# Kernel optimization log

Hardware: AMD Instinct MI355X
Metric: run time of the kernel (lower is better)

## Reference

```python
import jax, jax.numpy as jnp
import numpy as np

D_MODEL = 1024
NUM_HEADS = 16
HEAD_DIM = D_MODEL // NUM_HEADS


def setup_inputs() -> dict:
    key = jax.random.key(0)
    ks = jax.random.split(key, 12)
    B, S, D = 4, 2048, D_MODEL
    s = 1.0 / np.sqrt(D)
    return {
        "query": jax.random.normal(ks[0], (B, S, D), jnp.float32),
        "key": jax.random.normal(ks[1], (B, S, D), jnp.float32),
        "value": jax.random.normal(ks[2], (B, S, D), jnp.float32),
        "Wq": jax.random.normal(ks[3], (D, D), jnp.float32) * s,
        "bq": jax.random.normal(ks[4], (D,), jnp.float32) * 0.02,
        "Wk": jax.random.normal(ks[5], (D, D), jnp.float32) * s,
        "bk": jax.random.normal(ks[6], (D,), jnp.float32) * 0.02,
        "Wv": jax.random.normal(ks[7], (D, D), jnp.float32) * s,
        "bv": jax.random.normal(ks[8], (D,), jnp.float32) * 0.02,
        "Wo": jax.random.normal(ks[9], (D, D), jnp.float32) * s,
        "bo": jax.random.normal(ks[10], (D,), jnp.float32) * 0.02,
    }


def _split_heads(x):
    B, S, D = x.shape
    return x.reshape(B, S, NUM_HEADS, HEAD_DIM).transpose(0, 2, 1, 3)  # [B,H,S,hd]


def reference(query, key, value, Wq, bq, Wk, bk, Wv, bv, Wo, bo):
    q = _split_heads(query @ Wq + bq)
    k = _split_heads(key @ Wk + bk)
    v = _split_heads(value @ Wv + bv)
    # NOTE: original scales by 1/sqrt(d_model), not 1/sqrt(head_dim)
    scale = 1.0 / np.sqrt(D_MODEL).astype(np.float32)
    scores = jnp.einsum('bhqd,bhkd->bhqk', q, k) * scale  # [B,H,S,S]
    attn = jax.nn.softmax(scores, axis=-1)
    out = jnp.einsum('bhqk,bhkd->bhqd', attn, v)  # [B,H,S,hd]
    B, H, S, hd = out.shape
    out = out.transpose(0, 2, 1, 3).reshape(B, S, D_MODEL)
    out = out @ Wo + bo
    return out, attn
```

## Files before the change

### kernel.cpp

```cpp
#include <hip/hip_runtime.h>
#include <hip/hip_bf16.h>

typedef __bf16 bf16;
typedef __bf16 bf16x8 __attribute__((ext_vector_type(8)));
typedef __bf16 bf16x4 __attribute__((ext_vector_type(4)));
typedef __bf16 bf16x2 __attribute__((ext_vector_type(2)));
typedef float  f32x4  __attribute__((ext_vector_type(4)));
typedef float  f32x16 __attribute__((ext_vector_type(16)));
typedef unsigned int u32;

#define MFMA(A, B, C)   __builtin_amdgcn_mfma_f32_16x16x32_bf16((A), (B), (C), 0, 0, 0)
#define MFMA32(A, B, C) __builtin_amdgcn_mfma_f32_32x32x16_bf16((A), (B), (C), 0, 0, 0)

static constexpr int BATCH = 4, S = 2048, D = 1024, NH = 16, HD = 64;
static constexpr int M = BATCH * S;
static constexpr float KL = 0.045084220027780106f;

__device__ __forceinline__ void gload16(const void* g, void* l) {
  __builtin_amdgcn_global_load_lds(
      (const __attribute__((address_space(1))) void*)g,
      (__attribute__((address_space(3))) void*)l, 16, 0, 0);
}

__device__ __forceinline__ float fexp2(float x) {
#if __has_builtin(__builtin_amdgcn_exp2f)
  return __builtin_amdgcn_exp2f(x);
#else
  return exp2f(x);
#endif
}

__device__ __forceinline__ u32 pack2(float a, float b) {
  union { bf16x2 h; u32 u; } c;
  c.h = (bf16x2){(bf16)a, (bf16)b};
  return c.u;
}

union U4 { u32 w[4]; bf16x8 v; };

#define WAITV_BAR(n)                                        \
  asm volatile("s_waitcnt vmcnt(" #n ")" ::: "memory");     \
  __builtin_amdgcn_s_barrier();                             \
  __builtin_amdgcn_sched_barrier(0);

__global__ __launch_bounds__(256) void wt_convert(
    const float* __restrict__ W0, const float* __restrict__ W1,
    const float* __restrict__ W2, const float* __restrict__ W3,
    bf16* __restrict__ WtAll)
{
  const float* W = blockIdx.y == 0 ? W0 : blockIdx.y == 1 ? W1
                 : blockIdx.y == 2 ? W2 : W3;
  bf16* dst = WtAll + (size_t)blockIdx.y * (D * D);
  int k0 = (blockIdx.x >> 4) * 64, n0 = (blockIdx.x & 15) * 64;
  __shared__ __align__(16) bf16 T[64][72];
  int tid = threadIdx.x;
#pragma unroll
  for (int i = 0; i < 4; ++i) {
    int c = tid + i * 256, r = c >> 4, seg = c & 15;
    float4 v = *reinterpret_cast<const float4*>(W + (size_t)(k0 + r) * D + n0 + seg * 4);
    T[seg * 4 + 0][r] = (bf16)v.x; T[seg * 4 + 1][r] = (bf16)v.y;
    T[seg * 4 + 2][r] = (bf16)v.z; T[seg * 4 + 3][r] = (bf16)v.w;
  }
  __syncthreads();
#pragma unroll
  for (int i = 0; i < 2; ++i) {
    int c = tid + i * 256, r = c >> 3, seg = c & 7;
    *reinterpret_cast<bf16x8*>(dst + (size_t)(n0 + r) * D + k0 + seg * 8) =
        *reinterpret_cast<const bf16x8*>(&T[r][seg * 8]);
  }
}

__global__ __launch_bounds__(256) void x_convert(
    const float* __restrict__ X0, const float* __restrict__ X1,
    const float* __restrict__ X2, bf16* __restrict__ Y)
{
  int t = blockIdx.y;
  const float* X = t == 0 ? X0 : t == 1 ? X1 : X2;
  bf16* Yp = Y + (size_t)t * M * D;
  int idx = blockIdx.x * 256 + threadIdx.x;
#pragma unroll
  for (int i = 0; i < 4; ++i) {
    size_t j = (size_t)idx + (size_t)i * 524288;
    float4 v = reinterpret_cast<const float4*>(X)[j];
    bf16x4 o; o[0] = (bf16)v.x; o[1] = (bf16)v.y; o[2] = (bf16)v.z; o[3] = (bf16)v.w;
    reinterpret_cast<bf16x4*>(Yp)[j] = o;
  }
}

__global__ __launch_bounds__(256) void qkv_gemm(
    const bf16* __restrict__ Xb, const bf16* __restrict__ WtAll,
    const float* __restrict__ bq, const float* __restrict__ bk, const float* __restrict__ bv,
    bf16* __restrict__ Qb, bf16* __restrict__ Kb, bf16* __restrict__ Vtb)
{
  int v = blockIdx.y;
  const bf16*  X    = Xb + (size_t)v * M * D;
  const bf16*  Wt   = WtAll + (size_t)v * (D * D);
  const float* bias = v == 0 ? bq : v == 1 ? bk : bv;

  int x = blockIdx.x;
  int swz = (x & 7) * 64 + (x >> 3);
  int mt = swz >> 3, nt = swz & 7;
  int m0 = mt * 128, n0 = nt * 128;
  int tid = threadIdx.x, lane = tid & 63, w = tid >> 6;
  int wm = (w >> 1) * 64, wn = (w & 1) * 64;
  int lr = lane & 15, lg = lane >> 4;

  __shared__ __align__(16) unsigned char smem[34816];
  auto As = reinterpret_cast<bf16(*)[128][32]>(smem);
  auto Bs = reinterpret_cast<bf16(*)[128][32]>(smem + 16384);

  f32x4 acc[4][4] = {};

  int srow = w * 32 + (lane >> 2);
  int scol = (lane & 3) * 8;

  auto stage = [&](int buf, int ks) {
    const bf16* ga = X + (size_t)(m0 + srow) * D + ks * 32 + scol;
    bf16* la = &As[buf][w * 32][0];
    gload16(ga, la);
    gload16(ga + 16 * D, la + 16 * 32);
    const bf16* gb = Wt + (size_t)(n0 + srow) * D + ks * 32 + scol;
    bf16* lb = &Bs[buf][w * 32][0];
    gload16(gb, lb);
    gload16(gb + 16 * D, lb + 16 * 32);
  };

  stage(0, 0);
  for (int ks = 0; ks < 32; ++ks) {
    __syncthreads();
    if (ks < 31) stage((ks + 1) & 1, ks + 1);
    int buf = ks & 1;
    bf16x8 af[4], bfr[4];
#pragma unroll
    for (int i = 0; i < 4; ++i)
      af[i] = *reinterpret_cast<const bf16x8*>(&As[buf][wm + i * 16 + lr][8 * lg]);
#pragma unroll
    for (int j = 0; j < 4; ++j)
      bfr[j] = *reinterpret_cast<const bf16x8*>(&Bs[buf][wn + j * 16 + lr][8 * lg]);
#pragma unroll
    for (int i = 0; i < 4; ++i)
#pragma unroll
      for (int j = 0; j < 4; ++j)
        acc[i][j] = MFMA(af[i], bfr[j], acc[i][j]);
  }
  __syncthreads();

  if (v < 2) {
    bf16* Out = v == 0 ? Qb : Kb;
    float qs = v == 0 ? KL : 1.0f;
    auto Es = reinterpret_cast<bf16(*)[128]>(smem);
#pragma unroll
    for (int i = 0; i < 4; ++i)
#pragma unroll
      for (int j = 0; j < 4; ++j) {
        int n = wn + j * 16 + lr;
        float bias_n = bias[n0 + n];
#pragma unroll
        for (int r = 0; r < 4; ++r)
          Es[wm + i * 16 + 4 * lg + r][n] = (bf16)((acc[i][j][r] + bias_n) * qs);
      }
    __syncthreads();
#pragma unroll
    for (int i = 0; i < 8; ++i) {
      int c = tid + i * 256, r = c >> 4, seg = c & 15;
      int mg = m0 + r, b = mg >> 11, s = mg & 2047;
      int ng = n0 + seg * 8, h = ng >> 6, d = ng & 63;
      *reinterpret_cast<bf16x8*>(Out + (((size_t)(b * NH + h)) * S + s) * HD + d) =
          *reinterpret_cast<const bf16x8*>(&Es[r][seg * 8]);
    }
  } else {
    auto Es = reinterpret_cast<bf16(*)[136]>(smem);
#pragma unroll
    for (int i = 0; i < 4; ++i)
#pragma unroll
      for (int j = 0; j < 4; ++j) {
        int n = wn + j * 16 + lr;
        float bias_n = bias[n0 + n];
        bf16x4 t;
#pragma unroll
        for (int r = 0; r < 4; ++r) t[r] = (bf16)(acc[i][j][r] + bias_n);
        *reinterpret_cast<bf16x4*>(&Es[n][wm + i * 16 + 4 * lg]) = t;
      }
    __syncthreads();
#pragma unroll
    for (int i = 0; i < 8; ++i) {
      int c = tid + i * 256, r = c >> 4, seg = c & 15;
      int ng = n0 + r, h = ng >> 6, d = ng & 63;
      int mg = m0 + seg * 8, b = mg >> 11, s = mg & 2047;
      *reinterpret_cast<bf16x8*>(Vtb + (((size_t)(b * NH + h)) * HD + d) * S + s) =
          *reinterpret_cast<const bf16x8*>(&Es[r][seg * 8]);
    }
  }
}

__global__ __launch_bounds__(256) void attn_kernel(
    const bf16* __restrict__ Qb, const bf16* __restrict__ Kb, const bf16* __restrict__ Vtb,
    float* __restrict__ attn_out, bf16* __restrict__ ctx)
{
  int xx = blockIdx.x;
  int xcd = xx & 7, r8 = xx >> 3;
  int bh = xcd + 8 * (r8 >> 5);
  int qb = r8 & 31;
  int tid = threadIdx.x, lane = tid & 63, w = tid >> 6;
  int q32 = lane & 31, hi = lane >> 5;
  int qh = w & 1, kh = w >> 1;

  __shared__ __align__(16) bf16 Ks[2][64][64];
  __shared__ __align__(16) bf16 Vs[2][64][64];
  __shared__ __align__(16) float Ps[64][68];
  __shared__ float sums[2][64];

  int q_row = qb * 64 + qh * 32 + q32;
  const bf16* Qrow = Qb + ((size_t)bh * S + q_row) * HD;
  bf16x8 qreg[4];
#pragma unroll
  for (int c = 0; c < 4; ++c)
    qreg[c] = *reinterpret_cast<const bf16x8*>(Qrow + c * 16 + 8 * hi);

  auto stageK = [&](int buf, int kc) {
    const bf16* base = Kb + ((size_t)bh * S + kc * 64) * HD;
#pragma unroll
    for (int i = 0; i < 2; ++i) {
      int c = i * 256 + tid, row = c >> 3, j = c & 7;
      gload16(base + row * HD + 8 * (j ^ (row & 7)),
              reinterpret_cast<bf16*>(&Ks[buf][0][0]) + c * 8);
    }
  };
  auto stageV = [&](int buf, int kc) {
    const bf16* base = Vtb + (size_t)bh * HD * S + kc * 64;
#pragma unroll
    for (int i = 0; i < 2; ++i) {
      int c = i * 256 + tid, row = c >> 3, j = c & 7;
      gload16(base + (size_t)row * S + 8 * (j ^ (row & 7)),
              reinterpret_cast<bf16*>(&Vs[buf][0][0]) + c * 8);
    }
  };

  int krow = kh * 32 + q32, ks7 = krow & 7;

  float lrun = 0.f;
  stageK(0, 0);
  for (int kc = 0; kc < 32; ++kc) {
    if (kc < 31) {
      stageK((kc + 1) & 1, kc + 1);
      WAITV_BAR(2)
    } else {
      WAITV_BAR(0)
    }
    int buf = kc & 1;
    f32x16 sa = {};
#pragma unroll
    for (int c = 0; c < 4; ++c) {
      bf16x8 kf = *reinterpret_cast<const bf16x8*>(&Ks[buf][krow][8 * ((2 * c + hi) ^ ks7)]);
      sa = MFMA32(kf, qreg[c], sa);
    }
#pragma unroll
    for (int r = 0; r < 16; ++r) lrun += fexp2(sa[r]);
    __builtin_amdgcn_s_barrier();
  }
  lrun += __shfl_xor(lrun, 32);
  if (hi == 0) sums[kh][qh * 32 + q32] = lrun;
  __syncthreads();
  float lg2l = __log2f(sums[0][qh * 32 + q32] + sums[1][qh * 32 + q32]);

  f32x16 oaccA = {}, oaccB = {};
  float* ablk = attn_out + ((size_t)bh * S + qb * 64) * S;

  auto computeB = [&](int buf) {
    f32x16 sa = {};
#pragma unroll
    for (int c = 0; c < 4; ++c) {
      bf16x8 kf = *reinterpret_cast<const bf16x8*>(&Ks[buf][krow][8 * ((2 * c + hi) ^ ks7)]);
      sa = MFMA32(kf, qreg[c], sa);
    }
    u32 pku[8];
#pragma unroll
    for (int rq = 0; rq < 4; ++rq) {
      f32x4 pv;
#pragma unroll
      for (int j = 0; j < 4; ++j) pv[j] = fexp2(sa[rq * 4 + j] - lg2l);
      *reinterpret_cast<f32x4*>(&Ps[qh * 32 + q32][kh * 32 + 8 * rq + 4 * hi]) = pv;
      pku[rq * 2 + 0] = pack2(pv[0], pv[1]);
      pku[rq * 2 + 1] = pack2(pv[2], pv[3]);
    }
#pragma unroll
    for (int c2 = 0; c2 < 2; ++c2) {
      u32 myw0 = hi ? pku[4 * c2 + 2] : pku[4 * c2 + 0];
      u32 myw1 = hi ? pku[4 * c2 + 3] : pku[4 * c2 + 1];
      u32 sdw0 = hi ? pku[4 * c2 + 0] : pku[4 * c2 + 2];
      u32 sdw1 = hi ? pku[4 * c2 + 1] : pku[4 * c2 + 3];
      u32 r0 = __shfl_xor(sdw0, 32);
      u32 r1 = __shfl_xor(sdw1, 32);
      U4 f;
      f.w[0] = hi ? r0 : myw0;
      f.w[1] = hi ? r1 : myw1;
      f.w[2] = hi ? myw0 : r0;
      f.w[3] = hi ? myw1 : r1;
      {
        int vrow = q32, vs7 = vrow & 7;
        bf16x8 vf = *reinterpret_cast<const bf16x8*>(
            &Vs[buf][vrow][8 * ((4 * kh + 2 * c2 + hi) ^ vs7)]);
        oaccA = MFMA32(f.v, vf, oaccA);
      }
      {
        int vrow = 32 + q32, vs7 = vrow & 7;
        bf16x8 vf = *reinterpret_cast<const bf16x8*>(
            &Vs[buf][vrow][8 * ((4 * kh + 2 * c2 + hi) ^ vs7)]);
        oaccB = MFMA32(f.v, vf, oaccB);
      }
    }
  };

  int prow = tid >> 2, pc0 = (tid & 3) * 4;
  auto storeP = [&](int kc) {
    float* dst = ablk + (size_t)prow * S + kc * 64 + pc0;
#pragma unroll
    for (int i = 0; i < 4; ++i)
      __builtin_nontemporal_store(
          *reinterpret_cast<const f32x4*>(&Ps[prow][pc0 + 16 * i]),
          reinterpret_cast<f32x4*>(dst + 16 * i));
  };

  stageK(0, 0); stageV(0, 0);
  stageK(1, 1); stageV(1, 1);
  WAITV_BAR(4)
  computeB(0);
  __builtin_amdgcn_s_barrier();
  storeP(0);

  for (int kc = 1; kc < 32; ++kc) {
    if (kc < 31) {
      stageK((kc + 1) & 1, kc + 1);
      stageV((kc + 1) & 1, kc + 1);
      WAITV_BAR(8)
    } else {
      WAITV_BAR(4)
    }
    computeB(kc & 1);
    __builtin_amdgcn_s_barrier();
    storeP(kc);
  }

  float* fbuf = reinterpret_cast<float*>(&Ks[0][0][0]);
  if (kh == 1) {
#pragma unroll
    for (int reg = 0; reg < 16; ++reg) {
      int qloc = (reg & 3) + 8 * (reg >> 2) + 4 * hi;
      fbuf[(qh * 32 + qloc) * 64 + q32]      = oaccA[reg];
      fbuf[(qh * 32 + qloc) * 64 + 32 + q32] = oaccB[reg];
    }
  }
  __syncthreads();
  bf16* cs = reinterpret_cast<bf16*>(&Vs[0][0][0]);
  if (kh == 0) {
#pragma unroll
    for (int reg = 0; reg < 16; ++reg) {
      int qloc = (reg & 3) + 8 * (reg >> 2) + 4 * hi;
      cs[(qh * 32 + qloc) * 72 + q32] =
          (bf16)(oaccA[reg] + fbuf[(qh * 32 + qloc) * 64 + q32]);
      cs[(qh * 32 + qloc) * 72 + 32 + q32] =
          (bf16)(oaccB[reg] + fbuf[(qh * 32 + qloc) * 64 + 32 + q32]);
    }
  }
  __syncthreads();
  {
    int b = bh >> 4, h = bh & 15;
    int row = tid >> 2, cseg = (tid & 3) * 16;
    bf16* cp = ctx + ((size_t)b * S + qb * 64 + row) * D + h * HD + cseg;
    *reinterpret_cast<bf16x8*>(cp) =
        *reinterpret_cast<const bf16x8*>(&cs[row * 72 + cseg]);
    *reinterpret_cast<bf16x8*>(cp + 8) =
        *reinterpret_cast<const bf16x8*>(&cs[row * 72 + cseg + 8]);
  }
}

__global__ __launch_bounds__(256) void out_gemm(
    const bf16* __restrict__ ctx, const bf16* __restrict__ Wto,
    const float* __restrict__ bo, float* __restrict__ Out)
{
  int x = blockIdx.x;
  int swz = (x & 7) * 64 + (x >> 3);
  int mt = swz >> 3, nt = swz & 7;
  int m0 = mt * 128, n0 = nt * 128;
  int tid = threadIdx.x, lane = tid & 63, w = tid >> 6;
  int wm = (w >> 1) * 64, wn = (w & 1) * 64;
  int lr = lane & 15, lg = lane >> 4;

  __shared__ __align__(16) bf16 As[2][128][32];
  __shared__ __align__(16) bf16 Bs[2][128][32];

  f32x4 acc[4][4] = {};

  int srow = w * 32 + (lane >> 2);
  int scol = (lane & 3) * 8;

  auto stage = [&](int buf, int ks) {
    const bf16* ga = ctx + (size_t)(m0 + srow) * D + ks * 32 + scol;
    bf16* la = &As[buf][w * 32][0];
    gload16(ga, la);
    gload16(ga + 16 * D, la + 16 * 32);
    const bf16* gb = Wto + (size_t)(n0 + srow) * D + ks * 32 + scol;
    bf16* lb = &Bs[buf][w * 32][0];
    gload16(gb, lb);
    gload16(gb + 16 * D, lb + 16 * 32);
  };

  stage(0, 0);
  for (int ks = 0; ks < 32; ++ks) {
    __syncthreads();
    if (ks < 31) stage((ks + 1) & 1, ks + 1);
    int buf = ks & 1;
    bf16x8 af[4], bfr[4];
#pragma unroll
    for (int i = 0; i < 4; ++i)
      af[i] = *reinterpret_cast<const bf16x8*>(&As[buf][wm + i * 16 + lr][8 * lg]);
#pragma unroll
    for (int j = 0; j < 4; ++j)
      bfr[j] = *reinterpret_cast<const bf16x8*>(&Bs[buf][wn + j * 16 + lr][8 * lg]);
#pragma unroll
    for (int i = 0; i < 4; ++i)
#pragma unroll
      for (int j = 0; j < 4; ++j)
        acc[i][j] = MFMA(af[i], bfr[j], acc[i][j]);
  }

#pragma unroll
  for (int i = 0; i < 4; ++i)
#pragma unroll
    for (int j = 0; j < 4; ++j) {
      int n = n0 + wn + j * 16 + lr;
      float bias_n = bo[n];
#pragma unroll
      for (int r = 0; r < 4; ++r)
        Out[(size_t)(m0 + wm + i * 16 + 4 * lg + r) * D + n] = acc[i][j][r] + bias_n;
    }
}

extern "C" void kernel_launch(void* const* d_in, const int* in_sizes, int n_in,
                              void* d_out, int out_size, void* d_ws, size_t ws_size,
                              hipStream_t stream)
{
  const float* query = (const float*)d_in[0];
  const float* key   = (const float*)d_in[1];
  const float* value = (const float*)d_in[2];
  const float* Wq = (const float*)d_in[3]; const float* bq = (const float*)d_in[4];
  const float* Wk = (const float*)d_in[5]; const float* bk = (const float*)d_in[6];
  const float* Wv = (const float*)d_in[7]; const float* bv = (const float*)d_in[8];
  const float* Wo = (const float*)d_in[9]; const float* bo = (const float*)d_in[10];

  float* out  = (float*)d_out;
  float* attn = out + (size_t)M * D;

  char* ws = (char*)d_ws;
  const size_t MiB = 1048576;
  bf16* WtAll = (bf16*)ws;
  bf16* Xb    = (bf16*)(ws + 8 * MiB);
  bf16* Qb    = (bf16*)(ws + 56 * MiB);
  bf16* Kb    = (bf16*)(ws + 72 * MiB);
  bf16* Vtb   = (bf16*)(ws + 88 * MiB);
  bf16* ctx   = Xb;

  wt_convert<<<dim3(256, 4), 256, 0, stream>>>(Wq, Wk, Wv, Wo, WtAll);
  x_convert<<<dim3(2048, 3), 256, 0, stream>>>(query, key, value, Xb);
  qkv_gemm<<<dim3(512, 3), 256, 0, stream>>>(Xb, WtAll, bq, bk, bv, Qb, Kb, Vtb);
  attn_kernel<<<dim3(2048), 256, 0, stream>>>(Qb, Kb, Vtb, attn, ctx);
  out_gemm<<<dim3(512), 256, 0, stream>>>(ctx, WtAll + (size_t)3 * D * D, bo, out);
}
```

Before: 442.4 us.

## Process two query tiles per attention block, fusing second tile's sum pass

Each attention block now handles 128 query rows as two 64-row tiles. The softmax-denominator pass for the second tile is folded into the first tile's output pass, so the K tiles loaded there serve both tiles. This removes one of the four separate K sweeps per pair of tiles and halves the grid to 1024 blocks. The cost is more registers (two Q register sets, more accumulators), less parallelism across blocks, and extra barriers and lgkmcnt waits from the new fence macro.

```diff
diff --git a/kernel.cpp b/kernel.cpp
--- a/kernel.cpp
+++ b/kernel.cpp
@@ -38,9 +38,14 @@
 
 union U4 { u32 w[4]; bf16x8 v; };
 
-#define WAITV_BAR(n)                                        \
-  asm volatile("s_waitcnt vmcnt(" #n ")" ::: "memory");     \
-  __builtin_amdgcn_s_barrier();                             \
+#define WAITV_BAR(n)                                                     \
+  asm volatile("s_waitcnt vmcnt(" #n ") lgkmcnt(0)" ::: "memory");       \
+  __builtin_amdgcn_s_barrier();                                          \
+  __builtin_amdgcn_sched_barrier(0);
+
+#define FENCE_BAR                                                        \
+  asm volatile("s_waitcnt lgkmcnt(0)" ::: "memory");                     \
+  __builtin_amdgcn_s_barrier();                                          \
   __builtin_amdgcn_sched_barrier(0);
 
 __global__ __launch_bounds__(256) void wt_convert(
@@ -199,8 +204,8 @@
 {
   int xx = blockIdx.x;
   int xcd = xx & 7, r8 = xx >> 3;
-  int bh = xcd + 8 * (r8 >> 5);
-  int qb = r8 & 31;
+  int bh = xcd + 8 * (r8 >> 4);
+  int qp = r8 & 15;
   int tid = threadIdx.x, lane = tid & 63, w = tid >> 6;
   int q32 = lane & 31, hi = lane >> 5;
   int qh = w & 1, kh = w >> 1;
@@ -210,12 +215,15 @@
   __shared__ __align__(16) float Ps[64][68];
   __shared__ float sums[2][64];
 
-  int q_row = qb * 64 + qh * 32 + q32;
-  const bf16* Qrow = Qb + ((size_t)bh * S + q_row) * HD;
-  bf16x8 qreg[4];
-#pragma unroll
-  for (int c = 0; c < 4; ++c)
-    qreg[c] = *reinterpret_cast<const bf16x8*>(Qrow + c * 16 + 8 * hi);
+  int qrowX = qp * 128 + qh * 32 + q32;
+  const bf16* QrowX = Qb + ((size_t)bh * S + qrowX) * HD;
+  const bf16* QrowY = QrowX + (size_t)64 * HD;
+  bf16x8 qregX[4], qregY[4];
+#pragma unroll
+  for (int c = 0; c < 4; ++c) {
+    qregX[c] = *reinterpret_cast<const bf16x8*>(QrowX + c * 16 + 8 * hi);
+    qregY[c] = *reinterpret_cast<const bf16x8*>(QrowY + c * 16 + 8 * hi);
+  }
 
   auto stageK = [&](int buf, int kc) {
     const bf16* base = Kb + ((size_t)bh * S + kc * 64) * HD;
@@ -238,7 +246,7 @@
 
   int krow = kh * 32 + q32, ks7 = krow & 7;
 
-  float lrun = 0.f;
+  float xs[4] = {0.f, 0.f, 0.f, 0.f};
   stageK(0, 0);
   for (int kc = 0; kc < 32; ++kc) {
     if (kc < 31) {
@@ -252,37 +260,36 @@
 #pragma unroll
     for (int c = 0; c < 4; ++c) {
       bf16x8 kf = *reinterpret_cast<const bf16x8*>(&Ks[buf][krow][8 * ((2 * c + hi) ^ ks7)]);
-      sa = MFMA32(kf, qreg[c], sa);
-    }
-#pragma unroll
-    for (int r = 0; r < 16; ++r) lrun += fexp2(sa[r]);
-    __builtin_amdgcn_s_barrier();
-  }
-  lrun += __shfl_xor(lrun, 32);
-  if (hi == 0) sums[kh][qh * 32 + q32] = lrun;
+      sa = MFMA32(kf, qregX[c], sa);
+    }
+#pragma unroll
+    for (int r = 0; r < 16; ++r) xs[r & 3] += fexp2(sa[r]);
+    FENCE_BAR
+  }
+  {
+    float lrun = (xs[0] + xs[1]) + (xs[2] + xs[3]);
+    lrun += __shfl_xor(lrun, 32);
+    if (hi == 0) sums[kh][qh * 32 + q32] = lrun;
+  }
   __syncthreads();
-  float lg2l = __log2f(sums[0][qh * 32 + q32] + sums[1][qh * 32 + q32]);
+  float lg2lX = __log2f(sums[0][qh * 32 + q32] + sums[1][qh * 32 + q32]);
 
   f32x16 oaccA = {}, oaccB = {};
-  float* ablk = attn_out + ((size_t)bh * S + qb * 64) * S;
-
-  auto computeB = [&](int buf) {
-    f32x16 sa = {};
-#pragma unroll
-    for (int c = 0; c < 4; ++c) {
-      bf16x8 kf = *reinterpret_cast<const bf16x8*>(&Ks[buf][krow][8 * ((2 * c + hi) ^ ks7)]);
-      sa = MFMA32(kf, qreg[c], sa);
-    }
-    u32 pku[8];
-#pragma unroll
-    for (int rq = 0; rq < 4; ++rq) {
-      f32x4 pv;
-#pragma unroll
-      for (int j = 0; j < 4; ++j) pv[j] = fexp2(sa[rq * 4 + j] - lg2l);
-      *reinterpret_cast<f32x4*>(&Ps[qh * 32 + q32][kh * 32 + 8 * rq + 4 * hi]) = pv;
-      pku[rq * 2 + 0] = pack2(pv[0], pv[1]);
-      pku[rq * 2 + 1] = pack2(pv[2], pv[3]);
-    }
+  float ys[4] = {0.f, 0.f, 0.f, 0.f};
+  float* ablkX = attn_out + ((size_t)bh * S + qp * 128) * S;
+  float* ablkY = ablkX + (size_t)64 * S;
+  int prow = tid >> 2, pc0 = (tid & 3) * 4;
+
+  auto storeP = [&](float* ablk, int kc) {
+    float* dst = ablk + (size_t)prow * S + kc * 64 + pc0;
+#pragma unroll
+    for (int i = 0; i < 4; ++i)
+      __builtin_nontemporal_store(
+          *reinterpret_cast<const f32x4*>(&Ps[prow][pc0 + 16 * i]),
+          reinterpret_cast<f32x4*>(dst + 16 * i));
+  };
+
+  auto pv_accum = [&](int buf, const u32* pku) {
 #pragma unroll
     for (int c2 = 0; c2 < 2; ++c2) {
       u32 myw0 = hi ? pku[4 * c2 + 2] : pku[4 * c2 + 0];
@@ -311,23 +318,35 @@
     }
   };
 
-  int prow = tid >> 2, pc0 = (tid & 3) * 4;
-  auto storeP = [&](int kc) {
-    float* dst = ablk + (size_t)prow * S + kc * 64 + pc0;
-#pragma unroll
-    for (int i = 0; i < 4; ++i)
-      __builtin_nontemporal_store(
-          *reinterpret_cast<const f32x4*>(&Ps[prow][pc0 + 16 * i]),
-          reinterpret_cast<f32x4*>(dst + 16 * i));
+  auto merged = [&](int buf) {
+    f32x16 saX = {}, saY = {};
+#pragma unroll
+    for (int c = 0; c < 4; ++c) {
+      bf16x8 kf = *reinterpret_cast<const bf16x8*>(&Ks[buf][krow][8 * ((2 * c + hi) ^ ks7)]);
+      saX = MFMA32(kf, qregX[c], saX);
+      saY = MFMA32(kf, qregY[c], saY);
+    }
+    u32 pku[8];
+#pragma unroll
+    for (int rq = 0; rq < 4; ++rq) {
+      f32x4 pv;
+#pragma unroll
+      for (int j = 0; j < 4; ++j) pv[j] = fexp2(saX[rq * 4 + j] - lg2lX);
+      *reinterpret_cast<f32x4*>(&Ps[qh * 32 + q32][kh * 32 + 8 * rq + 4 * hi]) = pv;
+      pku[rq * 2 + 0] = pack2(pv[0], pv[1]);
+      pku[rq * 2 + 1] = pack2(pv[2], pv[3]);
+    }
+    pv_accum(buf, pku);
+#pragma unroll
+    for (int r = 0; r < 16; ++r) ys[r & 3] += fexp2(saY[r]);
   };
 
   stageK(0, 0); stageV(0, 0);
   stageK(1, 1); stageV(1, 1);
   WAITV_BAR(4)
-  computeB(0);
-  __builtin_amdgcn_s_barrier();
-  storeP(0);
-
+  merged(0);
+  FENCE_BAR
+  storeP(ablkX, 0);
   for (int kc = 1; kc < 32; ++kc) {
     if (kc < 31) {
       stageK((kc + 1) & 1, kc + 1);
@@ -336,42 +355,100 @@
     } else {
       WAITV_BAR(4)
     }
-    computeB(kc & 1);
-    __builtin_amdgcn_s_barrier();
-    storeP(kc);
-  }
-
-  float* fbuf = reinterpret_cast<float*>(&Ks[0][0][0]);
-  if (kh == 1) {
-#pragma unroll
-    for (int reg = 0; reg < 16; ++reg) {
-      int qloc = (reg & 3) + 8 * (reg >> 2) + 4 * hi;
-      fbuf[(qh * 32 + qloc) * 64 + q32]      = oaccA[reg];
-      fbuf[(qh * 32 + qloc) * 64 + 32 + q32] = oaccB[reg];
-    }
+    merged(kc & 1);
+    FENCE_BAR
+    storeP(ablkX, kc);
+  }
+
+  {
+    float lrY = (ys[0] + ys[1]) + (ys[2] + ys[3]);
+    lrY += __shfl_xor(lrY, 32);
+    if (hi == 0) sums[kh][qh * 32 + q32] = lrY;
   }
   __syncthreads();
-  bf16* cs = reinterpret_cast<bf16*>(&Vs[0][0][0]);
-  if (kh == 0) {
-#pragma unroll
-    for (int reg = 0; reg < 16; ++reg) {
-      int qloc = (reg & 3) + 8 * (reg >> 2) + 4 * hi;
-      cs[(qh * 32 + qloc) * 72 + q32] =
-          (bf16)(oaccA[reg] + fbuf[(qh * 32 + qloc) * 64 + q32]);
-      cs[(qh * 32 + qloc) * 72 + 32 + q32] =
-          (bf16)(oaccB[reg] + fbuf[(qh * 32 + qloc) * 64 + 32 + q32]);
-    }
-  }
-  __syncthreads();
-  {
+  float lg2lY = __log2f(sums[0][qh * 32 + q32] + sums[1][qh * 32 + q32]);
+
+  auto ctx_write = [&](int qgbase) {
+    __syncthreads();
+    if (kh == 1) {
+#pragma unroll
+      for (int reg = 0; reg < 16; ++reg) {
+        int qloc = (reg & 3) + 8 * (reg >> 2) + 4 * hi;
+        Ps[qh * 32 + qloc][q32]      = oaccA[reg];
+        Ps[qh * 32 + qloc][32 + q32] = oaccB[reg];
+      }
+    }
+    __syncthreads();
+    if (kh == 0) {
+#pragma unroll
+      for (int reg = 0; reg < 16; ++reg) {
+        int qloc = (reg & 3) + 8 * (reg >> 2) + 4 * hi;
+        Ps[qh * 32 + qloc][q32]      += oaccA[reg];
+        Ps[qh * 32 + qloc][32 + q32] += oaccB[reg];
+      }
+    }
+    __syncthreads();
     int b = bh >> 4, h = bh & 15;
     int row = tid >> 2, cseg = (tid & 3) * 16;
-    bf16* cp = ctx + ((size_t)b * S + qb * 64 + row) * D + h * HD + cseg;
-    *reinterpret_cast<bf16x8*>(cp) =
-        *reinterpret_cast<const bf16x8*>(&cs[row * 72 + cseg]);
-    *reinterpret_cast<bf16x8*>(cp + 8) =
-        *reinterpret_cast<const bf16x8*>(&cs[row * 72 + cseg + 8]);
-  }
+    f32x4 v0 = *reinterpret_cast<const f32x4*>(&Ps[row][cseg]);
+    f32x4 v1 = *reinterpret_cast<const f32x4*>(&Ps[row][cseg + 4]);
+    f32x4 v2 = *reinterpret_cast<const f32x4*>(&Ps[row][cseg + 8]);
+    f32x4 v3 = *reinterpret_cast<const f32x4*>(&Ps[row][cseg + 12]);
+    bf16x8 o0, o1;
+#pragma unroll
+    for (int j = 0; j < 4; ++j) {
+      o0[j] = (bf16)v0[j]; o0[4 + j] = (bf16)v1[j];
+      o1[j] = (bf16)v2[j]; o1[4 + j] = (bf16)v3[j];
+    }
+    bf16* cp = ctx + ((size_t)b * S + qgbase + row) * D + h * HD + cseg;
+    *reinterpret_cast<bf16x8*>(cp)     = o0;
+    *reinterpret_cast<bf16x8*>(cp + 8) = o1;
+  };
+
+  ctx_write(qp * 128);
+#pragma unroll
+  for (int r = 0; r < 16; ++r) { oaccA[r] = 0.f; oaccB[r] = 0.f; }
+
+  auto bodyY = [&](int buf) {
+    f32x16 saY = {};
+#pragma unroll
+    for (int c = 0; c < 4; ++c) {
+      bf16x8 kf = *reinterpret_cast<const bf16x8*>(&Ks[buf][krow][8 * ((2 * c + hi) ^ ks7)]);
+      saY = MFMA32(kf, qregY[c], saY);
+    }
+    u32 pku[8];
+#pragma unroll
+    for (int rq = 0; rq < 4; ++rq) {
+      f32x4 pv;
+#pragma unroll
+      for (int j = 0; j < 4; ++j) pv[j] = fexp2(saY[rq * 4 + j] - lg2lY);
+      *reinterpret_cast<f32x4*>(&Ps[qh * 32 + q32][kh * 32 + 8 * rq + 4 * hi]) = pv;
+      pku[rq * 2 + 0] = pack2(pv[0], pv[1]);
+      pku[rq * 2 + 1] = pack2(pv[2], pv[3]);
+    }
+    pv_accum(buf, pku);
+  };
+
+  stageK(0, 0); stageV(0, 0);
+  stageK(1, 1); stageV(1, 1);
+  WAITV_BAR(4)
+  bodyY(0);
+  FENCE_BAR
+  storeP(ablkY, 0);
+  for (int kc = 1; kc < 32; ++kc) {
+    if (kc < 31) {
+      stageK((kc + 1) & 1, kc + 1);
+      stageV((kc + 1) & 1, kc + 1);
+      WAITV_BAR(8)
+    } else {
+      WAITV_BAR(4)
+    }
+    bodyY(kc & 1);
+    FENCE_BAR
+    storeP(ablkY, kc);
+  }
+
+  ctx_write(qp * 128 + 64);
 }
 
 __global__ __launch_bounds__(256) void out_gemm(
@@ -463,6 +540,6 @@
   wt_convert<<<dim3(256, 4), 256, 0, stream>>>(Wq, Wk, Wv, Wo, WtAll);
   x_convert<<<dim3(2048, 3), 256, 0, stream>>>(query, key, value, Xb);
   qkv_gemm<<<dim3(512, 3), 256, 0, stream>>>(Xb, WtAll, bq, bk, bv, Qb, Kb, Vtb);
-  attn_kernel<<<dim3(2048), 256, 0, stream>>>(Qb, Kb, Vtb, attn, ctx);
+  attn_kernel<<<dim3(1024), 256, 0, stream>>>(Qb, Kb, Vtb, attn, ctx);
   out_gemm<<<dim3(512), 256, 0, stream>>>(ctx, WtAll + (size_t)3 * D * D, bo, out);
 }
```

Result: no change. 448.7 us (+1.4%).
